# Performance work log

Measured on AMD Instinct MI355X. Metric: run time of the kernel, lower is better.

The kernel has to match this reference:

```python
import jax, jax.numpy as jnp
import numpy as np

B, H, N, M, C = 64, 8, 16384, 64, 1024
IVH = 3 * M + 6  # per-head interface size: k(M), beta, g, s(3), gamma, e(M), a(M)


def setup_inputs() -> dict:
    key = jax.random.key(0)
    k1, k2, k3, k4 = jax.random.split(key, 4)
    return {
        "x": jax.random.normal(k1, (B, C), dtype=jnp.float32),
        "current_memory": jax.random.normal(k2, (B, N, M), dtype=jnp.float32),
        "w_prev": jax.random.uniform(k3, (B, H, N), dtype=jnp.float32),
        "W": jax.random.normal(k4, (C, H * IVH), dtype=jnp.float32) * (1.0 / np.sqrt(C)),
        "b": jnp.zeros((H * IVH,), dtype=jnp.float32),
    }


def reference(x, current_memory, w_prev, W, b):
    eps = 1e-16
    iv = (x @ W + b).reshape(B, H, IVH)
    k = iv[..., :M]                                   # [B,H,M] content key
    beta = jax.nn.softplus(iv[..., M])                # [B,H] key strength
    g = jax.nn.sigmoid(iv[..., M + 1])                # [B,H] interpolation gate
    s = jax.nn.softmax(iv[..., M + 2:M + 5], axis=-1) # [B,H,3] shift weights
    gamma = 1.0 + jax.nn.softplus(iv[..., M + 5])     # [B,H] sharpening
    e = jax.nn.sigmoid(iv[..., M + 6:2 * M + 6])      # [B,H,M] erase
    a = iv[..., 2 * M + 6:3 * M + 6]                  # [B,H,M] add

    # content addressing: cosine similarity of k against every memory row
    num = jnp.einsum('bhm,bnm->bhn', k, current_memory)
    den = (jnp.linalg.norm(k, axis=-1)[..., None]
           * jnp.linalg.norm(current_memory, axis=-1)[:, None, :] + eps)
    cos = num / den                                   # [B,H,N]
    wc = jax.nn.softmax(beta[..., None] * cos, axis=-1)

    # gated interpolation with previous weighting
    wg = g[..., None] * wc + (1.0 - g[..., None]) * w_prev

    # circular conv1d shift with 3-tap kernel (shifts -1, 0, +1)
    ws = (s[..., 0:1] * jnp.roll(wg, 1, axis=-1)
          + s[..., 1:2] * wg
          + s[..., 2:3] * jnp.roll(wg, -1, axis=-1))

    # sharpening (power normalize)
    wp = ws ** gamma[..., None]
    w = wp / (jnp.sum(wp, axis=-1, keepdims=True) + eps)

    # read
    read_data = jnp.einsum('bhn,bnm->bhm', w, current_memory)
    return (read_data, w, e, a)
```

## Files before the change

### kernel.cpp

```cpp
#include <hip/hip_runtime.h>
#include <cstdint>
#include <cstddef>

#define B_    64
#define H_    8
#define N_    16384
#define M_    64
#define C_    1024
#define IVH_  198
#define J_    1584
#define NCHUNK_ 64

__device__ __forceinline__ float softplus_f(float x) {
    return (x > 20.f) ? x : log1pf(__expf(x));
}
__device__ __forceinline__ float sigmoid_f(float x) {
    return 1.f / (1.f + __expf(-x));
}

template<int CTRL>
__device__ __forceinline__ float dppf(float x) {
    return __int_as_float(__builtin_amdgcn_update_dpp(
        0, __float_as_int(x), CTRL, 0xF, 0xF, true));
}
#define RED16(v) { v += dppf<0xB1>(v); v += dppf<0x4E>(v); \
                   v += dppf<0x128>(v); v += dppf<0x124>(v); }

__device__ __forceinline__ float sel8(const float p[8], int i) {
    float r01 = (i & 1) ? p[1] : p[0];
    float r23 = (i & 1) ? p[3] : p[2];
    float r45 = (i & 1) ? p[5] : p[4];
    float r67 = (i & 1) ? p[7] : p[6];
    float a = (i & 2) ? r23 : r01;
    float c = (i & 2) ? r67 : r45;
    return (i & 4) ? c : a;
}

__global__ __launch_bounds__(64) void k_gemm(const float* __restrict__ x,
                                             const float* __restrict__ W,
                                             float* __restrict__ iv) {
    int lane = threadIdx.x;
    int j = blockIdx.x * 64 + lane;
    bool valid = (j < J_);
    int b0 = blockIdx.y * 16;
    int c0 = blockIdx.z * 64;
    const float* xb = x + (size_t)b0 * C_;
    float acc[16];
    #pragma unroll
    for (int i = 0; i < 16; ++i) acc[i] = 0.f;
    #pragma unroll 8
    for (int c = c0; c < c0 + 64; ++c) {
        float wv = valid ? W[(size_t)c * J_ + j] : 0.f;
        #pragma unroll
        for (int bi = 0; bi < 16; ++bi)
            acc[bi] = fmaf(xb[(size_t)bi * C_ + c], wv, acc[bi]);
    }
    if (valid) {
        #pragma unroll
        for (int bi = 0; bi < 16; ++bi)
            atomicAdd(&iv[(size_t)(b0 + bi) * J_ + j], acc[bi]);
    }
}

__global__ __launch_bounds__(256, 4) void k_passA(
        const float* __restrict__ mem, const float* __restrict__ iv,
        const float* __restrict__ bias, float* __restrict__ z,
        float* __restrict__ pmax, float* __restrict__ psum) {
    __shared__ float zl[8 * 257];
    int t = threadIdx.x;
    int b = blockIdx.y;
    int n0 = blockIdx.x << 8;
    int w = t >> 6, lane = t & 63, sub = lane >> 4, mq = lane & 15;

    const float* ivb = iv + (size_t)b * J_;
    float4 kreg[8];
    float nq[8];
    #pragma unroll
    for (int h = 0; h < 8; ++h) {
        const float* ivh = ivb + h * IVH_;
        const float* bbh = bias + h * IVH_;
        float2 a0 = *(const float2*)(ivh + mq * 4);
        float2 a1 = *(const float2*)(ivh + mq * 4 + 2);
        float2 c0 = *(const float2*)(bbh + mq * 4);
        float2 c1 = *(const float2*)(bbh + mq * 4 + 2);
        float4 kv = make_float4(a0.x + c0.x, a0.y + c0.y, a1.x + c1.x, a1.y + c1.y);
        float q = kv.x * kv.x + kv.y * kv.y + kv.z * kv.z + kv.w * kv.w;
        RED16(q);
        nq[h] = q;
        kreg[h] = kv;
    }
    float kn[8];
    #pragma unroll
    for (int h = 0; h < 8; ++h) {
        kn[h] = sqrtf(nq[h]);
        float v0 = ivb[h * IVH_ + 64] + bias[h * IVH_ + 64];
        float s = softplus_f(v0) / kn[h];
        kreg[h].x *= s; kreg[h].y *= s; kreg[h].z *= s; kreg[h].w *= s;
    }
    float epsl = 1e-16f / sel8(kn, mq & 7);

    const float* mb = mem + ((size_t)b * N_ + n0) * M_;
    #pragma unroll
    for (int rr = 0; rr < 16; ++rr) {
        int row = (w << 6) + (rr << 2) + sub;
        float4 mv = *(const float4*)(mb + (size_t)row * M_ + mq * 4);
        float pr[9];
        #pragma unroll
        for (int h = 0; h < 8; ++h)
            pr[h] = kreg[h].x * mv.x + kreg[h].y * mv.y
                  + kreg[h].z * mv.z + kreg[h].w * mv.w;
        pr[8] = mv.x * mv.x + mv.y * mv.y + mv.z * mv.z + mv.w * mv.w;
        #pragma unroll
        for (int i = 0; i < 9; ++i) { float vv = pr[i]; RED16(vv); pr[i] = vv; }
        if (mq < 8) {
            float rn = sqrtf(pr[8]);
            zl[mq * 257 + row] = sel8(pr, mq) / (rn + epsl);
        }
    }
    __syncthreads();

    #pragma unroll
    for (int h = 0; h < 8; ++h)
        z[(((size_t)b * 8 + h) << 14) + n0 + t] = zl[h * 257 + t];

    #pragma unroll
    for (int q = 0; q < 2; ++q) {
        int h = w * 2 + q;
        float a0 = zl[h * 257 + lane],       a1 = zl[h * 257 + lane + 64];
        float a2 = zl[h * 257 + lane + 128], a3 = zl[h * 257 + lane + 192];
        float mx = fmaxf(fmaxf(a0, a1), fmaxf(a2, a3));
        #pragma unroll
        for (int o = 32; o > 0; o >>= 1) mx = fmaxf(mx, __shfl_down(mx, o, 64));
        mx = __shfl(mx, 0, 64);
        float se = __expf(a0 - mx) + __expf(a1 - mx) + __expf(a2 - mx) + __expf(a3 - mx);
        #pragma unroll
        for (int o = 32; o > 0; o >>= 1) se += __shfl_down(se, o, 64);
        if (lane == 0) {
            pmax[(((size_t)b * 8 + h) << 6) + blockIdx.x] = mx;
            psum[(((size_t)b * 8 + h) << 6) + blockIdx.x] = se;
        }
    }
}

__global__ __launch_bounds__(256, 4) void k_passB(
        const float* __restrict__ mem, const float* __restrict__ z,
        const float* __restrict__ wprev, const float* __restrict__ iv,
        const float* __restrict__ bias, const float* __restrict__ pmax,
        const float* __restrict__ psum, float* __restrict__ out_w,
        float* __restrict__ sumwp, float* __restrict__ readAcc) {
    __shared__ float smem[3072 + 2064 + 32];
    __shared__ float pl[64];
    float* wp_s  = smem;
    float* wgl   = smem + 3072;
    float* racc2 = smem + 3072;
    float* sums  = smem + 3072 + 2064;

    int t = threadIdx.x;
    int b  = (B_ - 1) - blockIdx.y;
    int ck = (NCHUNK_ - 1) - blockIdx.x;
    int n0 = ck << 8;
    int n = n0 + t;
    int w = t >> 6, lane = t & 63, sub = lane >> 4, mq = lane & 15;

    #pragma unroll
    for (int q = 0; q < 2; ++q) {
        int h = w * 2 + q;
        size_t bh = (size_t)b * 8 + h;
        float m = pmax[(bh << 6) + lane];
        float s = psum[(bh << 6) + lane];
        float mx = m;
        #pragma unroll
        for (int o = 32; o > 0; o >>= 1) mx = fmaxf(mx, __shfl_xor(mx, o, 64));
        float sc = s * __expf(m - mx);
        #pragma unroll
        for (int o = 32; o > 0; o >>= 1) sc += __shfl_xor(sc, o, 64);
        if (lane == 0) { pl[h * 8 + 0] = mx; pl[h * 8 + 1] = 1.f / sc; }
    }
    if (t < 8) {
        const float* ivh = iv + (size_t)b * J_ + t * IVH_;
        const float* bbh = bias + t * IVH_;
        float v1 = ivh[65] + bbh[65];
        float v2 = ivh[66] + bbh[66];
        float v3 = ivh[67] + bbh[67];
        float v4 = ivh[68] + bbh[68];
        float v5 = ivh[69] + bbh[69];
        float mx3 = fmaxf(v2, fmaxf(v3, v4));
        float e2 = __expf(v2 - mx3), e3 = __expf(v3 - mx3), e4 = __expf(v4 - mx3);
        float inv = 1.f / (e2 + e3 + e4);
        pl[t * 8 + 2] = sigmoid_f(v1);
        pl[t * 8 + 3] = e2 * inv;
        pl[t * 8 + 4] = e3 * inv;
        pl[t * 8 + 5] = e4 * inv;
        pl[t * 8 + 6] = 1.f + softplus_f(v5);
    }
    __syncthreads();

    #pragma unroll
    for (int h = 0; h < 8; ++h) {
        size_t bh = (size_t)b * 8 + h;
        float Mx = pl[h * 8 + 0], iS = pl[h * 8 + 1];
        float g = pl[h * 8 + 2];
        float wc = __expf(z[(bh << 14) + n] - Mx) * iS;
        wgl[h * 258 + t + 1] = fmaf(g, wc, (1.f - g) * wprev[(bh << 14) + n]);
    }
    if (t < 2) {
        int nh   = (t == 0) ? ((n0 + N_ - 1) & (N_ - 1)) : ((n0 + 256) & (N_ - 1));
        int slot = (t == 0) ? 0 : 257;
        #pragma unroll
        for (int h = 0; h < 8; ++h) {
            size_t bh = (size_t)b * 8 + h;
            float Mx = pl[h * 8 + 0], iS = pl[h * 8 + 1];
            float g = pl[h * 8 + 2];
            float wc = __expf(z[(bh << 14) + nh] - Mx) * iS;
            wgl[h * 258 + slot] = fmaf(g, wc, (1.f - g) * wprev[(bh << 14) + nh]);
        }
    }
    __syncthreads();

    float wpv[8];
    #pragma unroll
    for (int h = 0; h < 8; ++h) {
        size_t bh = (size_t)b * 8 + h;
        float s0 = pl[h * 8 + 3], s1 = pl[h * 8 + 4], s2 = pl[h * 8 + 5];
        float gam = pl[h * 8 + 6];
        float wsv = s0 * wgl[h * 258 + t] + s1 * wgl[h * 258 + t + 1]
                  + s2 * wgl[h * 258 + t + 2];
        float v = __powf(wsv, gam);
        wpv[h] = v;
        out_w[(bh << 14) + n] = v;
    }
    #pragma unroll
    for (int h = 0; h < 8; ++h) {
        float s = wpv[h];
        #pragma unroll
        for (int o = 32; o > 0; o >>= 1) s += __shfl_down(s, o, 64);
        if (lane == 0) sums[w * 8 + h] = s;
    }
    *(float4*)(wp_s + t * 12)     = make_float4(wpv[0], wpv[1], wpv[2], wpv[3]);
    *(float4*)(wp_s + t * 12 + 4) = make_float4(wpv[4], wpv[5], wpv[6], wpv[7]);
    __syncthreads();
    if (t < 8)
        atomicAdd(&sumwp[b * 8 + t], sums[t] + sums[8 + t] + sums[16 + t] + sums[24 + t]);

    float4 acc[8];
    #pragma unroll
    for (int h = 0; h < 8; ++h) acc[h] = make_float4(0.f, 0.f, 0.f, 0.f);
    const float* mb = mem + ((size_t)b * N_ + n0) * M_;
    #pragma unroll
    for (int rr = 0; rr < 16; ++rr) {
        int row = (w << 6) + (rr << 2) + sub;
        float4 mv = *(const float4*)(mb + (size_t)row * M_ + mq * 4);
        float4 wA = *(const float4*)(wp_s + row * 12);
        float4 wB = *(const float4*)(wp_s + row * 12 + 4);
        float wv8[8] = {wA.x, wA.y, wA.z, wA.w, wB.x, wB.y, wB.z, wB.w};
        #pragma unroll
        for (int h = 0; h < 8; ++h) {
            acc[h].x = fmaf(wv8[h], mv.x, acc[h].x);
            acc[h].y = fmaf(wv8[h], mv.y, acc[h].y);
            acc[h].z = fmaf(wv8[h], mv.z, acc[h].z);
            acc[h].w = fmaf(wv8[h], mv.w, acc[h].w);
        }
    }
    #pragma unroll
    for (int h = 0; h < 8; ++h) {
        #pragma unroll
        for (int o = 32; o >= 16; o >>= 1) {
            acc[h].x += __shfl_down(acc[h].x, o, 64);
            acc[h].y += __shfl_down(acc[h].y, o, 64);
            acc[h].z += __shfl_down(acc[h].z, o, 64);
            acc[h].w += __shfl_down(acc[h].w, o, 64);
        }
    }
    if (lane < 16) {
        #pragma unroll
        for (int h = 0; h < 8; ++h)
            *(float4*)(racc2 + ((w * 8 + h) << 6) + mq * 4) = acc[h];
    }
    __syncthreads();
    #pragma unroll
    for (int r = 0; r < 2; ++r) {
        int idx = r * 256 + t;
        float s = racc2[idx] + racc2[512 + idx] + racc2[1024 + idx] + racc2[1536 + idx];
        atomicAdd(&readAcc[(size_t)b * 512 + idx], s);
    }
}

__global__ void k_finish(float* __restrict__ out_w, const float* __restrict__ sumwp,
                         const float* __restrict__ readAcc, const float* __restrict__ iv,
                         const float* __restrict__ bias, float* __restrict__ out_rd,
                         float* __restrict__ out_e, float* __restrict__ out_a) {
    int t = threadIdx.x;
    size_t idx = (size_t)blockIdx.x * 256 + t;
    int bh = (int)(idx >> 12);
    float inv = 1.f / (sumwp[bh] + 1e-16f);
    float4* p = (float4*)out_w + idx;
    float4 v = *p;
    v.x *= inv; v.y *= inv; v.z *= inv; v.w *= inv;
    *p = v;
    if (blockIdx.x < 128) {
        int i = blockIdx.x * 256 + t;
        out_rd[i] = readAcc[i] / (sumwp[i >> 6] + 1e-16f);
    } else if (blockIdx.x < 256) {
        int i = (blockIdx.x - 128) * 256 + t;
        int bb = i >> 9, h = (i >> 6) & 7, m = i & 63;
        int off = h * IVH_ + 70 + m;
        out_e[i] = sigmoid_f(iv[(size_t)bb * J_ + off] + bias[off]);
    } else if (blockIdx.x < 384) {
        int i = (blockIdx.x - 256) * 256 + t;
        int bb = i >> 9, h = (i >> 6) & 7, m = i & 63;
        int off = h * IVH_ + 134 + m;
        out_a[i] = iv[(size_t)bb * J_ + off] + bias[off];
    }
}

extern "C" void kernel_launch(void* const* d_in, const int* in_sizes, int n_in,
                              void* d_out, int out_size, void* d_ws, size_t ws_size,
                              hipStream_t stream) {
    const float* x     = (const float*)d_in[0];
    const float* mem   = (const float*)d_in[1];
    const float* wprev = (const float*)d_in[2];
    const float* W     = (const float*)d_in[3];
    const float* bias  = (const float*)d_in[4];

    float* out   = (float*)d_out;
    float* out_rd = out;
    float* out_w  = out + 32768;
    float* out_e  = out + 32768 + 8388608;
    float* out_a  = out_e + 32768;

    float* ws      = (float*)d_ws;
    float* iv      = ws;
    float* sumwp   = iv + 101376;
    float* readAcc = sumwp + 512;
    float* zbuf    = readAcc + 32768;
    float* pmax    = zbuf + 8388608;
    float* psum    = pmax + 32768;

    hipMemsetAsync(iv, 0, (size_t)(101376 + 512 + 32768) * 4, stream);

    k_gemm  <<<dim3(25, 4, 16), 64, 0, stream>>>(x, W, iv);
    k_passA <<<dim3(NCHUNK_, B_), 256, 0, stream>>>(mem, iv, bias, zbuf, pmax, psum);
    k_passB <<<dim3(NCHUNK_, B_), 256, 0, stream>>>(mem, zbuf, wprev, iv, bias,
                                                    pmax, psum, out_w, sumwp, readAcc);
    k_finish<<<8192, 256, 0, stream>>>(out_w, sumwp, readAcc, iv, bias,
                                       out_rd, out_e, out_a);
}
```

Baseline: 570.9 us.

## Fuse attention passes into one cooperative persistent kernel with grid syncs

Merges pass A, pass B and the finish step into a single cooperative kernel of 1024 blocks. Each block handles four 256-row chunks of one batch, and grid.sync replaces the kernel boundaries. Pass B now accumulates the read vector and the power sums in registers across its chunks, which cuts the number of atomics. Phase A switches from 16-lane DPP reductions to 8-lane shuffle reductions, and the GEMM K-split is halved. The cost is fewer blocks in flight, grid-wide barriers, and a three-kernel fallback path used if the cooperative launch fails.

```diff
diff --git a/kernel.cpp b/kernel.cpp
--- a/kernel.cpp
+++ b/kernel.cpp
@@ -1,6 +1,9 @@
 #include <hip/hip_runtime.h>
+#include <hip/hip_cooperative_groups.h>
 #include <cstdint>
 #include <cstddef>
+
+namespace cg = cooperative_groups;
 
 #define B_    64
 #define H_    8
@@ -17,15 +20,6 @@
 __device__ __forceinline__ float sigmoid_f(float x) {
     return 1.f / (1.f + __expf(-x));
 }
-
-template<int CTRL>
-__device__ __forceinline__ float dppf(float x) {
-    return __int_as_float(__builtin_amdgcn_update_dpp(
-        0, __float_as_int(x), CTRL, 0xF, 0xF, true));
-}
-#define RED16(v) { v += dppf<0xB1>(v); v += dppf<0x4E>(v); \
-                   v += dppf<0x128>(v); v += dppf<0x124>(v); }
-
 __device__ __forceinline__ float sel8(const float p[8], int i) {
     float r01 = (i & 1) ? p[1] : p[0];
     float r23 = (i & 1) ? p[3] : p[2];
@@ -43,13 +37,13 @@
     int j = blockIdx.x * 64 + lane;
     bool valid = (j < J_);
     int b0 = blockIdx.y * 16;
-    int c0 = blockIdx.z * 64;
+    int c0 = blockIdx.z * 128;
     const float* xb = x + (size_t)b0 * C_;
     float acc[16];
     #pragma unroll
     for (int i = 0; i < 16; ++i) acc[i] = 0.f;
-    #pragma unroll 8
-    for (int c = c0; c < c0 + 64; ++c) {
+    #pragma unroll 2
+    for (int c = c0; c < c0 + 128; ++c) {
         float wv = valid ? W[(size_t)c * J_ + j] : 0.f;
         #pragma unroll
         for (int bi = 0; bi < 16; ++bi)
@@ -62,109 +56,96 @@
     }
 }
 
-__global__ __launch_bounds__(256, 4) void k_passA(
+#define SMEM_FLOATS 5232
+
+__device__ __forceinline__ void phaseA_body(
+        int b, int ci0, int t, float* smem,
         const float* __restrict__ mem, const float* __restrict__ iv,
         const float* __restrict__ bias, float* __restrict__ z,
         float* __restrict__ pmax, float* __restrict__ psum) {
-    __shared__ float zl[8 * 257];
-    int t = threadIdx.x;
-    int b = blockIdx.y;
-    int n0 = blockIdx.x << 8;
-    int w = t >> 6, lane = t & 63, sub = lane >> 4, mq = lane & 15;
+    float* zl = smem;
+    int w = t >> 6, lane = t & 63;
+    int sub8 = lane >> 3, mq8 = lane & 7;
 
     const float* ivb = iv + (size_t)b * J_;
-    float4 kreg[8];
-    float nq[8];
+    float4 ka[8], kb[8];
+    float kn[8];
     #pragma unroll
     for (int h = 0; h < 8; ++h) {
-        const float* ivh = ivb + h * IVH_;
-        const float* bbh = bias + h * IVH_;
-        float2 a0 = *(const float2*)(ivh + mq * 4);
-        float2 a1 = *(const float2*)(ivh + mq * 4 + 2);
-        float2 c0 = *(const float2*)(bbh + mq * 4);
-        float2 c1 = *(const float2*)(bbh + mq * 4 + 2);
-        float4 kv = make_float4(a0.x + c0.x, a0.y + c0.y, a1.x + c1.x, a1.y + c1.y);
-        float q = kv.x * kv.x + kv.y * kv.y + kv.z * kv.z + kv.w * kv.w;
-        RED16(q);
-        nq[h] = q;
-        kreg[h] = kv;
-    }
-    float kn[8];
-    #pragma unroll
-    for (int h = 0; h < 8; ++h) {
-        kn[h] = sqrtf(nq[h]);
+        const float* ivh = ivb + h * IVH_ + mq8 * 8;
+        const float* bbh = bias + h * IVH_ + mq8 * 8;
+        float e0 = ivh[0]+bbh[0], e1 = ivh[1]+bbh[1], e2 = ivh[2]+bbh[2], e3 = ivh[3]+bbh[3];
+        float e4 = ivh[4]+bbh[4], e5 = ivh[5]+bbh[5], e6 = ivh[6]+bbh[6], e7 = ivh[7]+bbh[7];
+        float q = e0*e0+e1*e1+e2*e2+e3*e3+e4*e4+e5*e5+e6*e6+e7*e7;
+        q += __shfl_xor(q, 1, 64);
+        q += __shfl_xor(q, 2, 64);
+        q += __shfl_xor(q, 4, 64);
+        kn[h] = sqrtf(q);
         float v0 = ivb[h * IVH_ + 64] + bias[h * IVH_ + 64];
         float s = softplus_f(v0) / kn[h];
-        kreg[h].x *= s; kreg[h].y *= s; kreg[h].z *= s; kreg[h].w *= s;
-    }
-    float epsl = 1e-16f / sel8(kn, mq & 7);
-
-    const float* mb = mem + ((size_t)b * N_ + n0) * M_;
-    #pragma unroll
-    for (int rr = 0; rr < 16; ++rr) {
-        int row = (w << 6) + (rr << 2) + sub;
-        float4 mv = *(const float4*)(mb + (size_t)row * M_ + mq * 4);
-        float pr[9];
+        ka[h] = make_float4(e0*s, e1*s, e2*s, e3*s);
+        kb[h] = make_float4(e4*s, e5*s, e6*s, e7*s);
+    }
+    float epsl = 1e-16f / sel8(kn, mq8);
+
+    #pragma unroll 1
+    for (int kc = 0; kc < 4; ++kc) {
+        int ck = ci0 * 4 + kc;
+        int n0 = ck << 8;
+        const float* mb = mem + ((size_t)b * N_ + n0) * M_;
+        #pragma unroll
+        for (int rr = 0; rr < 8; ++rr) {
+            int row = (w << 6) + (rr << 3) + sub8;
+            const float* mr = mb + (size_t)row * M_ + mq8 * 8;
+            float4 m0 = *(const float4*)(mr);
+            float4 m1 = *(const float4*)(mr + 4);
+            float pr[9];
+            #pragma unroll
+            for (int h = 0; h < 8; ++h)
+                pr[h] = ka[h].x*m0.x + ka[h].y*m0.y + ka[h].z*m0.z + ka[h].w*m0.w
+                      + kb[h].x*m1.x + kb[h].y*m1.y + kb[h].z*m1.z + kb[h].w*m1.w;
+            pr[8] = m0.x*m0.x+m0.y*m0.y+m0.z*m0.z+m0.w*m0.w
+                  + m1.x*m1.x+m1.y*m1.y+m1.z*m1.z+m1.w*m1.w;
+            #pragma unroll
+            for (int o = 1; o < 8; o <<= 1) {
+                #pragma unroll
+                for (int i = 0; i < 9; ++i) pr[i] += __shfl_xor(pr[i], o, 64);
+            }
+            float rn = sqrtf(pr[8]);
+            zl[mq8 * 264 + row] = sel8(pr, mq8) / (rn + epsl);
+        }
+        __syncthreads();
         #pragma unroll
         for (int h = 0; h < 8; ++h)
-            pr[h] = kreg[h].x * mv.x + kreg[h].y * mv.y
-                  + kreg[h].z * mv.z + kreg[h].w * mv.w;
-        pr[8] = mv.x * mv.x + mv.y * mv.y + mv.z * mv.z + mv.w * mv.w;
-        #pragma unroll
-        for (int i = 0; i < 9; ++i) { float vv = pr[i]; RED16(vv); pr[i] = vv; }
-        if (mq < 8) {
-            float rn = sqrtf(pr[8]);
-            zl[mq * 257 + row] = sel8(pr, mq) / (rn + epsl);
-        }
-    }
-    __syncthreads();
-
-    #pragma unroll
-    for (int h = 0; h < 8; ++h)
-        z[(((size_t)b * 8 + h) << 14) + n0 + t] = zl[h * 257 + t];
-
-    #pragma unroll
-    for (int q = 0; q < 2; ++q) {
-        int h = w * 2 + q;
-        float a0 = zl[h * 257 + lane],       a1 = zl[h * 257 + lane + 64];
-        float a2 = zl[h * 257 + lane + 128], a3 = zl[h * 257 + lane + 192];
-        float mx = fmaxf(fmaxf(a0, a1), fmaxf(a2, a3));
-        #pragma unroll
-        for (int o = 32; o > 0; o >>= 1) mx = fmaxf(mx, __shfl_down(mx, o, 64));
-        mx = __shfl(mx, 0, 64);
-        float se = __expf(a0 - mx) + __expf(a1 - mx) + __expf(a2 - mx) + __expf(a3 - mx);
-        #pragma unroll
-        for (int o = 32; o > 0; o >>= 1) se += __shfl_down(se, o, 64);
-        if (lane == 0) {
-            pmax[(((size_t)b * 8 + h) << 6) + blockIdx.x] = mx;
-            psum[(((size_t)b * 8 + h) << 6) + blockIdx.x] = se;
-        }
-    }
-}
-
-__global__ __launch_bounds__(256, 4) void k_passB(
-        const float* __restrict__ mem, const float* __restrict__ z,
-        const float* __restrict__ wprev, const float* __restrict__ iv,
-        const float* __restrict__ bias, const float* __restrict__ pmax,
-        const float* __restrict__ psum, float* __restrict__ out_w,
-        float* __restrict__ sumwp, float* __restrict__ readAcc) {
-    __shared__ float smem[3072 + 2064 + 32];
-    __shared__ float pl[64];
-    float* wp_s  = smem;
-    float* wgl   = smem + 3072;
-    float* racc2 = smem + 3072;
-    float* sums  = smem + 3072 + 2064;
-
-    int t = threadIdx.x;
-    int b  = (B_ - 1) - blockIdx.y;
-    int ck = (NCHUNK_ - 1) - blockIdx.x;
-    int n0 = ck << 8;
-    int n = n0 + t;
-    int w = t >> 6, lane = t & 63, sub = lane >> 4, mq = lane & 15;
-
-    #pragma unroll
-    for (int q = 0; q < 2; ++q) {
-        int h = w * 2 + q;
+            z[(((size_t)b * 8 + h) << 14) + n0 + t] = zl[h * 264 + t];
+        #pragma unroll
+        for (int q2 = 0; q2 < 2; ++q2) {
+            int h = w * 2 + q2;
+            float a0 = zl[h * 264 + lane],       a1 = zl[h * 264 + lane + 64];
+            float a2 = zl[h * 264 + lane + 128], a3 = zl[h * 264 + lane + 192];
+            float mx = fmaxf(fmaxf(a0, a1), fmaxf(a2, a3));
+            #pragma unroll
+            for (int o = 32; o > 0; o >>= 1) mx = fmaxf(mx, __shfl_xor(mx, o, 64));
+            float se = __expf(a0 - mx) + __expf(a1 - mx) + __expf(a2 - mx) + __expf(a3 - mx);
+            #pragma unroll
+            for (int o = 32; o > 0; o >>= 1) se += __shfl_xor(se, o, 64);
+            if (lane == 0) {
+                pmax[(((size_t)b * 8 + h) << 6) + ck] = mx;
+                psum[(((size_t)b * 8 + h) << 6) + ck] = se;
+            }
+        }
+        __syncthreads();
+    }
+}
+
+__device__ __forceinline__ void phaseS_body(
+        int b, int t, float* pl,
+        const float* __restrict__ pmax, const float* __restrict__ psum,
+        const float* __restrict__ iv, const float* __restrict__ bias) {
+    int w = t >> 6, lane = t & 63;
+    #pragma unroll
+    for (int q2 = 0; q2 < 2; ++q2) {
+        int h = w * 2 + q2;
         size_t bh = (size_t)b * 8 + h;
         float m = pmax[(bh << 6) + lane];
         float s = psum[(bh << 6) + lane];
@@ -194,72 +175,89 @@
         pl[t * 8 + 6] = 1.f + softplus_f(v5);
     }
     __syncthreads();
-
-    #pragma unroll
-    for (int h = 0; h < 8; ++h) {
-        size_t bh = (size_t)b * 8 + h;
-        float Mx = pl[h * 8 + 0], iS = pl[h * 8 + 1];
-        float g = pl[h * 8 + 2];
-        float wc = __expf(z[(bh << 14) + n] - Mx) * iS;
-        wgl[h * 258 + t + 1] = fmaf(g, wc, (1.f - g) * wprev[(bh << 14) + n]);
-    }
-    if (t < 2) {
-        int nh   = (t == 0) ? ((n0 + N_ - 1) & (N_ - 1)) : ((n0 + 256) & (N_ - 1));
-        int slot = (t == 0) ? 0 : 257;
+}
+
+__device__ __forceinline__ void phaseB_body(
+        int b, int ci0, int t, float* smem, const float* pl,
+        const float* __restrict__ mem, const float* __restrict__ z,
+        const float* __restrict__ wprev, float* __restrict__ out_w,
+        float* __restrict__ sumwp, float* __restrict__ readAcc) {
+    float* wp_s  = smem;
+    float* wgl   = smem + 3072;
+    float* racc2 = smem + 3072;
+    float* sums  = smem + 5136;
+    int w = t >> 6, lane = t & 63, sub = lane >> 4, mq = lane & 15;
+
+    float4 acc[8];
+    #pragma unroll
+    for (int h = 0; h < 8; ++h) acc[h] = make_float4(0.f, 0.f, 0.f, 0.f);
+    float ssum[8] = {0.f,0.f,0.f,0.f,0.f,0.f,0.f,0.f};
+
+    #pragma unroll 1
+    for (int kc = 0; kc < 4; ++kc) {
+        int ck = ci0 * 4 + kc;
+        int n0 = ck << 8;
+        int n = n0 + t;
         #pragma unroll
         for (int h = 0; h < 8; ++h) {
             size_t bh = (size_t)b * 8 + h;
-            float Mx = pl[h * 8 + 0], iS = pl[h * 8 + 1];
-            float g = pl[h * 8 + 2];
-            float wc = __expf(z[(bh << 14) + nh] - Mx) * iS;
-            wgl[h * 258 + slot] = fmaf(g, wc, (1.f - g) * wprev[(bh << 14) + nh]);
-        }
-    }
-    __syncthreads();
-
-    float wpv[8];
+            float Mx = pl[h * 8 + 0], iS = pl[h * 8 + 1], g = pl[h * 8 + 2];
+            float wc = __expf(z[(bh << 14) + n] - Mx) * iS;
+            wgl[h * 258 + t + 1] = fmaf(g, wc, (1.f - g) * wprev[(bh << 14) + n]);
+        }
+        if (t < 2) {
+            int nh   = (t == 0) ? ((n0 + N_ - 1) & (N_ - 1)) : ((n0 + 256) & (N_ - 1));
+            int slot = (t == 0) ? 0 : 257;
+            #pragma unroll
+            for (int h = 0; h < 8; ++h) {
+                size_t bh = (size_t)b * 8 + h;
+                float Mx = pl[h * 8 + 0], iS = pl[h * 8 + 1], g = pl[h * 8 + 2];
+                float wc = __expf(z[(bh << 14) + nh] - Mx) * iS;
+                wgl[h * 258 + slot] = fmaf(g, wc, (1.f - g) * wprev[(bh << 14) + nh]);
+            }
+        }
+        __syncthreads();
+        float wpv[8];
+        #pragma unroll
+        for (int h = 0; h < 8; ++h) {
+            size_t bh = (size_t)b * 8 + h;
+            float s0 = pl[h * 8 + 3], s1 = pl[h * 8 + 4], s2 = pl[h * 8 + 5];
+            float gam = pl[h * 8 + 6];
+            float wsv = s0 * wgl[h * 258 + t] + s1 * wgl[h * 258 + t + 1]
+                      + s2 * wgl[h * 258 + t + 2];
+            float v = __powf(wsv, gam);
+            wpv[h] = v;
+            ssum[h] += v;
+            out_w[(bh << 14) + n] = v;
+        }
+        *(float4*)(wp_s + t * 12)     = make_float4(wpv[0], wpv[1], wpv[2], wpv[3]);
+        *(float4*)(wp_s + t * 12 + 4) = make_float4(wpv[4], wpv[5], wpv[6], wpv[7]);
+        __syncthreads();
+        const float* mb = mem + ((size_t)b * N_ + n0) * M_;
+        #pragma unroll
+        for (int rr = 0; rr < 16; ++rr) {
+            int row = (w << 6) + (rr << 2) + sub;
+            float4 mv = *(const float4*)(mb + (size_t)row * M_ + mq * 4);
+            float4 wA = *(const float4*)(wp_s + row * 12);
+            float4 wB = *(const float4*)(wp_s + row * 12 + 4);
+            float wv8[8] = {wA.x, wA.y, wA.z, wA.w, wB.x, wB.y, wB.z, wB.w};
+            #pragma unroll
+            for (int h = 0; h < 8; ++h) {
+                acc[h].x = fmaf(wv8[h], mv.x, acc[h].x);
+                acc[h].y = fmaf(wv8[h], mv.y, acc[h].y);
+                acc[h].z = fmaf(wv8[h], mv.z, acc[h].z);
+                acc[h].w = fmaf(wv8[h], mv.w, acc[h].w);
+            }
+        }
+        __syncthreads();
+    }
+
     #pragma unroll
     for (int h = 0; h < 8; ++h) {
-        size_t bh = (size_t)b * 8 + h;
-        float s0 = pl[h * 8 + 3], s1 = pl[h * 8 + 4], s2 = pl[h * 8 + 5];
-        float gam = pl[h * 8 + 6];
-        float wsv = s0 * wgl[h * 258 + t] + s1 * wgl[h * 258 + t + 1]
-                  + s2 * wgl[h * 258 + t + 2];
-        float v = __powf(wsv, gam);
-        wpv[h] = v;
-        out_w[(bh << 14) + n] = v;
-    }
-    #pragma unroll
-    for (int h = 0; h < 8; ++h) {
-        float s = wpv[h];
+        float s = ssum[h];
         #pragma unroll
         for (int o = 32; o > 0; o >>= 1) s += __shfl_down(s, o, 64);
         if (lane == 0) sums[w * 8 + h] = s;
-    }
-    *(float4*)(wp_s + t * 12)     = make_float4(wpv[0], wpv[1], wpv[2], wpv[3]);
-    *(float4*)(wp_s + t * 12 + 4) = make_float4(wpv[4], wpv[5], wpv[6], wpv[7]);
-    __syncthreads();
-    if (t < 8)
-        atomicAdd(&sumwp[b * 8 + t], sums[t] + sums[8 + t] + sums[16 + t] + sums[24 + t]);
-
-    float4 acc[8];
-    #pragma unroll
-    for (int h = 0; h < 8; ++h) acc[h] = make_float4(0.f, 0.f, 0.f, 0.f);
-    const float* mb = mem + ((size_t)b * N_ + n0) * M_;
-    #pragma unroll
-    for (int rr = 0; rr < 16; ++rr) {
-        int row = (w << 6) + (rr << 2) + sub;
-        float4 mv = *(const float4*)(mb + (size_t)row * M_ + mq * 4);
-        float4 wA = *(const float4*)(wp_s + row * 12);
-        float4 wB = *(const float4*)(wp_s + row * 12 + 4);
-        float wv8[8] = {wA.x, wA.y, wA.z, wA.w, wB.x, wB.y, wB.z, wB.w};
-        #pragma unroll
-        for (int h = 0; h < 8; ++h) {
-            acc[h].x = fmaf(wv8[h], mv.x, acc[h].x);
-            acc[h].y = fmaf(wv8[h], mv.y, acc[h].y);
-            acc[h].z = fmaf(wv8[h], mv.z, acc[h].z);
-            acc[h].w = fmaf(wv8[h], mv.w, acc[h].w);
-        }
     }
     #pragma unroll
     for (int h = 0; h < 8; ++h) {
@@ -277,6 +275,8 @@
             *(float4*)(racc2 + ((w * 8 + h) << 6) + mq * 4) = acc[h];
     }
     __syncthreads();
+    if (t < 8)
+        atomicAdd(&sumwp[b * 8 + t], sums[t] + sums[8 + t] + sums[16 + t] + sums[24 + t]);
     #pragma unroll
     for (int r = 0; r < 2; ++r) {
         int idx = r * 256 + t;
@@ -285,32 +285,95 @@
     }
 }
 
-__global__ void k_finish(float* __restrict__ out_w, const float* __restrict__ sumwp,
-                         const float* __restrict__ readAcc, const float* __restrict__ iv,
-                         const float* __restrict__ bias, float* __restrict__ out_rd,
-                         float* __restrict__ out_e, float* __restrict__ out_a) {
+__device__ __forceinline__ void phaseF_body(
+        int b, int ci0, int t, float* pl,
+        float* __restrict__ out_w, const float* __restrict__ sumwp,
+        const float* __restrict__ readAcc, const float* __restrict__ iv,
+        const float* __restrict__ bias, float* __restrict__ out_rd,
+        float* __restrict__ out_e, float* __restrict__ out_a) {
+    if (t < 8) pl[t] = 1.f / (sumwp[b * 8 + t] + 1e-16f);
+    __syncthreads();
+    #pragma unroll 1
+    for (int kc = 0; kc < 4; ++kc) {
+        int n0 = (ci0 * 4 + kc) << 8;
+        #pragma unroll
+        for (int h = 0; h < 8; ++h) {
+            size_t idx = (((size_t)b * 8 + h) << 14) + n0 + t;
+            out_w[idx] *= pl[h];
+        }
+    }
+    if (ci0 == 0) {
+        #pragma unroll
+        for (int r = 0; r < 2; ++r) {
+            int i = r * 256 + t;
+            int gi = b * 512 + i;
+            out_rd[gi] = readAcc[gi] * pl[i >> 6];
+            int h = i >> 6, m = i & 63;
+            int offe = h * IVH_ + 70 + m;
+            out_e[gi] = sigmoid_f(iv[(size_t)b * J_ + offe] + bias[offe]);
+            int offa = h * IVH_ + 134 + m;
+            out_a[gi] = iv[(size_t)b * J_ + offa] + bias[offa];
+        }
+    }
+}
+
+__global__ __launch_bounds__(256, 4) void k_fused(
+        const float* __restrict__ mem, const float* __restrict__ wprev,
+        const float* __restrict__ iv, const float* __restrict__ bias,
+        float* __restrict__ z, float* __restrict__ pmax, float* __restrict__ psum,
+        float* __restrict__ out_w, float* __restrict__ sumwp,
+        float* __restrict__ readAcc, float* __restrict__ out_rd,
+        float* __restrict__ out_e, float* __restrict__ out_a) {
+    __shared__ float smem[SMEM_FLOATS];
+    float* pl = smem + 5168;
+    cg::grid_group grid = cg::this_grid();
+
     int t = threadIdx.x;
-    size_t idx = (size_t)blockIdx.x * 256 + t;
-    int bh = (int)(idx >> 12);
-    float inv = 1.f / (sumwp[bh] + 1e-16f);
-    float4* p = (float4*)out_w + idx;
-    float4 v = *p;
-    v.x *= inv; v.y *= inv; v.z *= inv; v.w *= inv;
-    *p = v;
-    if (blockIdx.x < 128) {
-        int i = blockIdx.x * 256 + t;
-        out_rd[i] = readAcc[i] / (sumwp[i >> 6] + 1e-16f);
-    } else if (blockIdx.x < 256) {
-        int i = (blockIdx.x - 128) * 256 + t;
-        int bb = i >> 9, h = (i >> 6) & 7, m = i & 63;
-        int off = h * IVH_ + 70 + m;
-        out_e[i] = sigmoid_f(iv[(size_t)bb * J_ + off] + bias[off]);
-    } else if (blockIdx.x < 384) {
-        int i = (blockIdx.x - 256) * 256 + t;
-        int bb = i >> 9, h = (i >> 6) & 7, m = i & 63;
-        int off = h * IVH_ + 134 + m;
-        out_a[i] = iv[(size_t)bb * J_ + off] + bias[off];
-    }
+    int b   = (int)(blockIdx.x >> 4);
+    int ci0 = (int)(blockIdx.x & 15);
+
+    phaseA_body(b, ci0, t, smem, mem, iv, bias, z, pmax, psum);
+    __threadfence();
+    grid.sync();
+    phaseS_body(b, t, pl, pmax, psum, iv, bias);
+    phaseB_body(b, ci0, t, smem, pl, mem, z, wprev, out_w, sumwp, readAcc);
+    __threadfence();
+    grid.sync();
+    phaseF_body(b, ci0, t, pl, out_w, sumwp, readAcc, iv, bias, out_rd, out_e, out_a);
+}
+
+__global__ __launch_bounds__(256, 4) void k_A(
+        const float* __restrict__ mem, const float* __restrict__ iv,
+        const float* __restrict__ bias, float* __restrict__ z,
+        float* __restrict__ pmax, float* __restrict__ psum) {
+    __shared__ float smem[SMEM_FLOATS];
+    int t = threadIdx.x;
+    phaseA_body((int)(blockIdx.x >> 4), (int)(blockIdx.x & 15), t, smem,
+                mem, iv, bias, z, pmax, psum);
+}
+__global__ __launch_bounds__(256, 4) void k_B(
+        const float* __restrict__ mem, const float* __restrict__ wprev,
+        const float* __restrict__ iv, const float* __restrict__ bias,
+        const float* __restrict__ z, const float* __restrict__ pmax,
+        const float* __restrict__ psum, float* __restrict__ out_w,
+        float* __restrict__ sumwp, float* __restrict__ readAcc) {
+    __shared__ float smem[SMEM_FLOATS];
+    float* pl = smem + 5168;
+    int t = threadIdx.x;
+    int b = (int)(blockIdx.x >> 4), ci0 = (int)(blockIdx.x & 15);
+    phaseS_body(b, t, pl, pmax, psum, iv, bias);
+    phaseB_body(b, ci0, t, smem, pl, mem, z, wprev, out_w, sumwp, readAcc);
+}
+__global__ __launch_bounds__(256, 4) void k_F(
+        float* __restrict__ out_w, const float* __restrict__ sumwp,
+        const float* __restrict__ readAcc, const float* __restrict__ iv,
+        const float* __restrict__ bias, float* __restrict__ out_rd,
+        float* __restrict__ out_e, float* __restrict__ out_a) {
+    __shared__ float smem[SMEM_FLOATS];
+    float* pl = smem + 5168;
+    int t = threadIdx.x;
+    phaseF_body((int)(blockIdx.x >> 4), (int)(blockIdx.x & 15), t, pl,
+                out_w, sumwp, readAcc, iv, bias, out_rd, out_e, out_a);
 }
 
 extern "C" void kernel_launch(void* const* d_in, const int* in_sizes, int n_in,
@@ -322,7 +385,7 @@
     const float* W     = (const float*)d_in[3];
     const float* bias  = (const float*)d_in[4];
 
-    float* out   = (float*)d_out;
+    float* out    = (float*)d_out;
     float* out_rd = out;
     float* out_w  = out + 32768;
     float* out_e  = out + 32768 + 8388608;
@@ -338,10 +401,19 @@
 
     hipMemsetAsync(iv, 0, (size_t)(101376 + 512 + 32768) * 4, stream);
 
-    k_gemm  <<<dim3(25, 4, 16), 64, 0, stream>>>(x, W, iv);
-    k_passA <<<dim3(NCHUNK_, B_), 256, 0, stream>>>(mem, iv, bias, zbuf, pmax, psum);
-    k_passB <<<dim3(NCHUNK_, B_), 256, 0, stream>>>(mem, zbuf, wprev, iv, bias,
-                                                    pmax, psum, out_w, sumwp, readAcc);
-    k_finish<<<8192, 256, 0, stream>>>(out_w, sumwp, readAcc, iv, bias,
-                                       out_rd, out_e, out_a);
-}
+    k_gemm<<<dim3(25, 4, 8), 64, 0, stream>>>(x, W, iv);
+
+    void* args[] = {(void*)&mem, (void*)&wprev, (void*)&iv, (void*)&bias,
+                    (void*)&zbuf, (void*)&pmax, (void*)&psum, (void*)&out_w,
+                    (void*)&sumwp, (void*)&readAcc, (void*)&out_rd,
+                    (void*)&out_e, (void*)&out_a};
+    hipError_t err = hipLaunchCooperativeKernel((void*)k_fused, dim3(1024), dim3(256),
+                                                args, 0, stream);
+    if (err != hipSuccess) {
+        k_A<<<1024, 256, 0, stream>>>(mem, iv, bias, zbuf, pmax, psum);
+        k_B<<<1024, 256, 0, stream>>>(mem, wprev, iv, bias, zbuf, pmax, psum,
+                                      out_w, sumwp, readAcc);
+        k_F<<<1024, 256, 0, stream>>>(out_w, sumwp, readAcc, iv, bias,
+                                      out_rd, out_e, out_a);
+    }
+}
```

Measured after the change: 1.091 ms. 1.91x slower.
